# Performance work log

Measured on AMD Instinct MI355X. Metric: run time of the kernel, lower is better.

## Reference

```python
import jax, jax.numpy as jnp
import numpy as np

GRID_SIZE = 5
SPLINE_ORDER = 3
GRID_RANGE = (-1.0, 1.0)


def b_splines(x, grid, spline_order=SPLINE_ORDER):
    # x: [B, in], grid: [G] with G = grid_size + 2*spline_order + 1
    x = x[..., None]                      # [B, in, 1]
    g = grid[None, None, :]               # [1, 1, G]
    bases = ((x >= g[..., :-1]) & (x < g[..., 1:])).astype(x.dtype)  # [B, in, G-1]
    for k in range(1, spline_order + 1):
        left = (x - g[..., :-(k + 1)]) / (g[..., k:-1] - g[..., :-(k + 1)]) * bases[..., :-1]
        right = (g[..., k + 1:] - x) / (g[..., k + 1:] - g[..., 1:-k]) * bases[..., 1:]
        bases = left + right
    return bases                          # [B, in, grid_size + spline_order]


def setup_inputs() -> dict:
    key = jax.random.key(0)
    k1, k2, k3, k4 = jax.random.split(key, 4)
    B, IN, OUT = 32768, 256, 256
    n_coef = GRID_SIZE + SPLINE_ORDER  # 8
    h = (GRID_RANGE[1] - GRID_RANGE[0]) / GRID_SIZE
    grid = jnp.arange(-SPLINE_ORDER, GRID_SIZE + SPLINE_ORDER + 1, dtype=jnp.float32) * h + GRID_RANGE[0]  # [12]
    x = jax.random.normal(k1, (B, IN), dtype=jnp.float32)
    base_weight = jax.random.normal(k2, (OUT, IN), dtype=jnp.float32) * np.sqrt(2.0 / IN)
    spline_weight = jax.random.normal(k3, (OUT, IN, n_coef), dtype=jnp.float32) * (0.1 / GRID_SIZE)
    spline_scaler = jax.random.normal(k4, (OUT, IN), dtype=jnp.float32) * np.sqrt(2.0 / IN)
    return {"x": x, "base_weight": base_weight, "spline_weight": spline_weight,
            "spline_scaler": spline_scaler, "grid": grid}


def reference(x, base_weight, spline_weight, spline_scaler, grid):
    B = x.shape[0]
    out_features = base_weight.shape[0]
    # base branch: silu(x) @ base_weight^T
    base_out = jnp.matmul(jax.nn.silu(x), base_weight.T)  # [B, out]
    # spline branch
    bases = b_splines(x, grid)                             # [B, in, n_coef]
    scaled_w = spline_weight * spline_scaler[..., None]    # [out, in, n_coef]
    spline_out = jnp.matmul(bases.reshape(B, -1), scaled_w.reshape(out_features, -1).T)
    return base_out + spline_out
```

## Files before the change

kernel.cpp:

```cpp
#include <hip/hip_runtime.h>
#include <stdint.h>


#define IN_F 256
#define OUT_F 256
#define KDIM 2304
#define BK 64
#define NCHUNK (KDIM / BK)

typedef float f32x4 __attribute__((ext_vector_type(4)));
typedef short bf16x8 __attribute__((ext_vector_type(8)));

__device__ __forceinline__ uint32_t f2bf(float f) {
    union { float f; uint32_t u; } c; c.f = f;
    uint32_t u = c.u;
    return (u + 0x7FFFu + ((u >> 16) & 1u)) >> 16;
}

__device__ __forceinline__ uint32_t cvtpk(float lo, float hi) {
    uint32_t r;
    asm("v_cvt_pk_bf16_f32 %0, %1, %2" : "=v"(r) : "v"(lo), "v"(hi));
    return r;
}

__device__ __forceinline__ float silu_f(float v) {
    return v / (1.0f + __expf(-v));
}

__device__ __forceinline__ void block_sync_lds() {
    __builtin_amdgcn_sched_barrier(0);
    asm volatile("s_waitcnt lgkmcnt(0)" ::: "memory");
    __builtin_amdgcn_sched_barrier(0);
    __builtin_amdgcn_s_barrier();
    __builtin_amdgcn_sched_barrier(0);
}

__device__ __forceinline__ uint4 basis16(float xx) {
    float u = __builtin_fmaf(xx, 2.5f, 5.5f);
    float jf = floorf(u);
    float t = u - jf;
    int j0 = (int)jf;
    float t2 = t * t, t3 = t2 * t;
    float p3 = t3 * (1.0f / 6.0f);
    float p2 = __builtin_fmaf(t3, -0.5f,
               __builtin_fmaf(t2, 0.5f, __builtin_fmaf(t, 0.5f, 1.0f / 6.0f)));
    float p1 = __builtin_fmaf(t3, 0.5f, __builtin_fmaf(t2, -1.0f, 2.0f / 3.0f));
    float omt = 1.0f - t;
    float p0 = omt * omt * omt * (1.0f / 6.0f);
    const int s0 = j0 - 3;
    int ds = s0 >> 1;
    if ((unsigned)j0 > 10u) ds = 9;
    const bool odd = (s0 & 1) != 0;
    uint32_t v0 = cvtpk(odd ? 0.0f : p0, odd ? p0 : p1);
    uint32_t v1 = cvtpk(odd ? p1 : p2, odd ? p2 : p3);
    uint32_t v2 = odd ? cvtpk(p3, 0.0f) : 0u;
    uint4 r;
    r.x = (ds == 0) ? v0 : (ds == -1) ? v1 : (ds == -2) ? v2 : 0u;
    r.y = (ds == 1) ? v0 : (ds ==  0) ? v1 : (ds == -1) ? v2 : 0u;
    r.z = (ds == 2) ? v0 : (ds ==  1) ? v1 : (ds ==  0) ? v2 : 0u;
    r.w = (ds == 3) ? v0 : (ds ==  2) ? v1 : (ds ==  1) ? v2 : 0u;
    return r;
}

__device__ __forceinline__ size_t wcf_addr(int col, int k) {
    const int kc = k >> 6, kkh = (k >> 5) & 1, q = (k >> 3) & 3, e = k & 7;
    return ((size_t)((kc * 2 + kkh) * 16 + (col >> 4))) * 512 +
           (size_t)(q * 16 + (col & 15)) * 8 + e;
}

__global__ void build_w(const float* __restrict__ bw, const float* __restrict__ sw,
                        const float* __restrict__ ss, unsigned short* __restrict__ WcF) {
    const int o = blockIdx.x;
    const int i = threadIdx.x;
    WcF[wcf_addr(o, i)] = (unsigned short)f2bf(bw[o * IN_F + i]);
    const float scal = ss[o * IN_F + i];
    const float4* swv = reinterpret_cast<const float4*>(sw + (size_t)(o * IN_F + i) * 8);
    float4 s0 = swv[0], s1 = swv[1];
    uint4 wv;
    wv.x = f2bf(s0.x * scal) | (f2bf(s0.y * scal) << 16);
    wv.y = f2bf(s0.z * scal) | (f2bf(s0.w * scal) << 16);
    wv.z = f2bf(s1.x * scal) | (f2bf(s1.y * scal) << 16);
    wv.w = f2bf(s1.z * scal) | (f2bf(s1.w * scal) << 16);
    *reinterpret_cast<uint4*>(WcF + wcf_addr(o, IN_F + i * 8)) = wv;
}

__launch_bounds__(512, 2)
__global__ void kan_fused(const float* __restrict__ x, const unsigned short* __restrict__ WcF,
                          float* __restrict__ out) {
    __shared__ __align__(16) unsigned short As[4][64 * 64];

    const int bid = blockIdx.x;
    const int row0 = bid * 64;
    const int tid = threadIdx.x;
    const int lane = tid & 63;
    const int w = tid >> 6;
    const int kh = w >> 2;
    const int wn = w & 3;
    const int l15 = lane & 15;
    const int q = lane >> 4;

    const int erow = tid >> 3;
    const int g8   = tid & 7;

    f32x4 acc[4][4] = {};
    bf16x8 bE[4], bO[4];
    float x0, x1, x2, x3;

    const unsigned short* wbase = WcF + (size_t)lane * 8;

    auto load_b = [&](int kc, bf16x8* dst) {
#pragma unroll
        for (int nt = 0; nt < 4; ++nt)
            dst[nt] = *reinterpret_cast<const bf16x8*>(
                wbase + ((size_t)((kc * 2 + kh) * 16 + wn * 4 + nt)) * 512);
    };
    auto load_x_silu = [&](int c, float4& a, float4& b) {
        const float* xp = x + (size_t)(row0 + erow) * IN_F + c * 64 + g8 * 8;
        a = reinterpret_cast<const float4*>(xp)[0];
        b = reinterpret_cast<const float4*>(xp)[1];
    };
    auto load_x_bas = [&](int c, float& v) {
        v = x[(size_t)(row0 + erow) * IN_F + (c - 4) * 8 + g8];
    };
    auto expand_silu = [&](float4 a, float4 b, uint4& w0) {
        w0.x = cvtpk(silu_f(a.x), silu_f(a.y));
        w0.y = cvtpk(silu_f(a.z), silu_f(a.w));
        w0.z = cvtpk(silu_f(b.x), silu_f(b.y));
        w0.w = cvtpk(silu_f(b.z), silu_f(b.w));
    };
    auto write_a = [&](unsigned short* Ab, const uint4& w0) {
        *reinterpret_cast<uint4*>(Ab + erow * 64 + ((g8 ^ (erow & 7)) << 3)) = w0;
    };
    auto mfma_chunk = [&](const unsigned short* Ab, const bf16x8* bv) {
        const int g0 = kh * 4 + q;
#pragma unroll
        for (int mt = 0; mt < 4; ++mt) {
            int r = mt * 16 + l15;
            bf16x8 a = *reinterpret_cast<const bf16x8*>(
                Ab + r * 64 + ((g0 ^ (r & 7)) << 3));
            __builtin_amdgcn_s_setprio(1);
#pragma unroll
            for (int nt = 0; nt < 4; ++nt)
                acc[mt][nt] = __builtin_amdgcn_mfma_f32_16x16x32_bf16(
                    a, bv[nt], acc[mt][nt], 0, 0, 0);
            __builtin_amdgcn_s_setprio(0);
        }
    };

    float4 s2a, s2b, s3a, s3b;
    {
        float4 a, b; uint4 t;
        load_x_silu(0, a, b);
        load_x_silu(1, s2a, s2b);
        load_x_silu(2, s3a, s3b);
        load_b(0, bE);
        load_x_bas(4, x0);
        load_x_bas(5, x1);
        expand_silu(a, b, t);          write_a(&As[0][0], t);
        expand_silu(s2a, s2b, t);      write_a(&As[1][0], t);
        load_x_silu(3, s2a, s2b);
    }
    block_sync_lds();

    load_b(1, bO);
    {
        uint4 a2, a3;
        expand_silu(s3a, s3b, a2);
        expand_silu(s2a, s2b, a3);
        write_a(&As[2][0], a2);
        write_a(&As[3][0], a3);
    }
    mfma_chunk(&As[0][0], bE);
    load_b(2, bE);
    mfma_chunk(&As[1][0], bO);
    block_sync_lds();

    for (int t = 0; t < 8; ++t) {
        {
            const int kc = 4 * t + 2;
            load_b(kc + 1, bO);
            load_x_bas(kc + 4, x2);
            load_x_bas(kc + 5, x3);
            uint4 wa0, wa1;
            if (kh == 0) {
                wa0 = basis16(x0); wa1 = basis16(x1);
                write_a(&As[0][0], wa0); write_a(&As[1][0], wa1);
                mfma_chunk(&As[2][0], bE);
                load_b(kc + 2, bE);
                mfma_chunk(&As[3][0], bO);
            } else {
                mfma_chunk(&As[2][0], bE);
                load_b(kc + 2, bE);
                mfma_chunk(&As[3][0], bO);
                wa0 = basis16(x0); wa1 = basis16(x1);
                write_a(&As[0][0], wa0); write_a(&As[1][0], wa1);
            }
            block_sync_lds();
        }
        {
            const int kc2 = 4 * t + 4;
            load_b(kc2 + 1, bO);
            if (kc2 + 5 < NCHUNK) {
                load_x_bas(kc2 + 4, x0);
                load_x_bas(kc2 + 5, x1);
            }
            uint4 wa0, wa1;
            if (kh == 0) {
                wa0 = basis16(x2); wa1 = basis16(x3);
                write_a(&As[2][0], wa0); write_a(&As[3][0], wa1);
                mfma_chunk(&As[0][0], bE);
                load_b(kc2 + 2, bE);
                mfma_chunk(&As[1][0], bO);
            } else {
                mfma_chunk(&As[0][0], bE);
                load_b(kc2 + 2, bE);
                mfma_chunk(&As[1][0], bO);
                wa0 = basis16(x2); wa1 = basis16(x3);
                write_a(&As[2][0], wa0); write_a(&As[3][0], wa1);
            }
            block_sync_lds();
        }
    }

    load_b(35, bO);
    mfma_chunk(&As[2][0], bE);
    mfma_chunk(&As[3][0], bO);

    float* red = reinterpret_cast<float*>(&As[0][0]);
    const int slot = wn & 1;
    auto ridx = [&](int row, int col) {
        return row * 64 + (col ^ ((((row) >> 2) & 3) << 4));
    };
#pragma unroll
    for (int round = 0; round < 2; ++round) {
        block_sync_lds();
        if ((wn >> 1) == round && kh == 1) {
#pragma unroll
            for (int mt = 0; mt < 4; ++mt)
#pragma unroll
                for (int nt = 0; nt < 4; ++nt)
#pragma unroll
                    for (int r = 0; r < 4; ++r)
                        red[slot * 4096 + ridx(mt * 16 + q * 4 + r, nt * 16 + l15)] =
                            acc[mt][nt][r];
        }
        block_sync_lds();
        if ((wn >> 1) == round && kh == 0) {
#pragma unroll
            for (int mt = 0; mt < 4; ++mt)
#pragma unroll
                for (int nt = 0; nt < 4; ++nt)
#pragma unroll
                    for (int r = 0; r < 4; ++r) {
                        float v = acc[mt][nt][r] +
                                  red[slot * 4096 + ridx(mt * 16 + q * 4 + r, nt * 16 + l15)];
                        out[(size_t)(row0 + mt * 16 + q * 4 + r) * OUT_F +
                            wn * 64 + nt * 16 + l15] = v;
                    }
        }
    }
}

extern "C" void kernel_launch(void* const* d_in, const int* in_sizes, int n_in,
                              void* d_out, int out_size, void* d_ws, size_t ws_size,
                              hipStream_t stream) {
    const float* x  = (const float*)d_in[0];
    const float* bw = (const float*)d_in[1];
    const float* sw = (const float*)d_in[2];
    const float* ss = (const float*)d_in[3];
    unsigned short* WcF = (unsigned short*)d_ws;

    build_w<<<dim3(OUT_F), dim3(IN_F), 0, stream>>>(bw, sw, ss, WcF);

    const int B_ROWS = in_sizes[0] / IN_F;
    kan_fused<<<dim3(B_ROWS / 64), dim3(512), 0, stream>>>(
        x, WcF, (float*)d_out);
}
```

Before: 138.7 us.

## Build MFMA A-operands directly in registers instead of staging through LDS

Each lane now loads the x values matching its own MFMA A-fragment straight from global memory and computes the silu or B-spline basis in registers, then feeds the result to the MFMA. This removes the LDS staging buffers and the per-chunk block barriers. LDS is now used only for the final cross-wave reduction. In exchange, the 8 waves redundantly recompute overlapping basis and silu values and issue more scattered, smaller global loads of x.

```diff
diff --git a/kernel.cpp b/kernel.cpp
--- a/kernel.cpp
+++ b/kernel.cpp
@@ -87,7 +87,7 @@
 __launch_bounds__(512, 2)
 __global__ void kan_fused(const float* __restrict__ x, const unsigned short* __restrict__ WcF,
                           float* __restrict__ out) {
-    __shared__ __align__(16) unsigned short As[4][64 * 64];
+    __shared__ __align__(16) float red[2][64 * 64];
 
     const int bid = blockIdx.x;
     const int row0 = bid * 64;
@@ -99,14 +99,18 @@
     const int l15 = lane & 15;
     const int q = lane >> 4;
 
-    const int erow = tid >> 3;
-    const int g8   = tid & 7;
+    const int fOff = kh * 4 + q;
+    const int koff = fOff * 8;
 
     f32x4 acc[4][4] = {};
     bf16x8 bE[4], bO[4];
-    float x0, x1, x2, x3;
+    float xE[4], xO[4];
 
     const unsigned short* wbase = WcF + (size_t)lane * 8;
+    const float* xr[4];
+#pragma unroll
+    for (int mt = 0; mt < 4; ++mt)
+        xr[mt] = x + (size_t)(row0 + mt * 16 + l15) * IN_F;
 
     auto load_b = [&](int kc, bf16x8* dst) {
 #pragma unroll
@@ -114,122 +118,65 @@
             dst[nt] = *reinterpret_cast<const bf16x8*>(
                 wbase + ((size_t)((kc * 2 + kh) * 16 + wn * 4 + nt)) * 512);
     };
-    auto load_x_silu = [&](int c, float4& a, float4& b) {
-        const float* xp = x + (size_t)(row0 + erow) * IN_F + c * 64 + g8 * 8;
-        a = reinterpret_cast<const float4*>(xp)[0];
-        b = reinterpret_cast<const float4*>(xp)[1];
-    };
-    auto load_x_bas = [&](int c, float& v) {
-        v = x[(size_t)(row0 + erow) * IN_F + (c - 4) * 8 + g8];
-    };
-    auto expand_silu = [&](float4 a, float4 b, uint4& w0) {
-        w0.x = cvtpk(silu_f(a.x), silu_f(a.y));
-        w0.y = cvtpk(silu_f(a.z), silu_f(a.w));
-        w0.z = cvtpk(silu_f(b.x), silu_f(b.y));
-        w0.w = cvtpk(silu_f(b.z), silu_f(b.w));
-    };
-    auto write_a = [&](unsigned short* Ab, const uint4& w0) {
-        *reinterpret_cast<uint4*>(Ab + erow * 64 + ((g8 ^ (erow & 7)) << 3)) = w0;
-    };
-    auto mfma_chunk = [&](const unsigned short* Ab, const bf16x8* bv) {
-        const int g0 = kh * 4 + q;
+    auto load_x = [&](int c, float* xs) {
+#pragma unroll
+        for (int mt = 0; mt < 4; ++mt)
+            xs[mt] = xr[mt][(c - 4) * 8 + fOff];
+    };
+    auto mfma4 = [&](int mt, bf16x8 a, const bf16x8* bv) {
+        __builtin_amdgcn_s_setprio(1);
+#pragma unroll
+        for (int nt = 0; nt < 4; ++nt)
+            acc[mt][nt] = __builtin_amdgcn_mfma_f32_16x16x32_bf16(
+                a, bv[nt], acc[mt][nt], 0, 0, 0);
+        __builtin_amdgcn_s_setprio(0);
+    };
+
+    load_b(0, bE);
+    load_x(4, xE);
+#pragma unroll
+    for (int c = 0; c < 4; ++c) {
+        bf16x8* bcur = (c & 1) ? bO : bE;
+        bf16x8* bnxt = (c & 1) ? bE : bO;
+        load_b(c + 1, bnxt);
 #pragma unroll
         for (int mt = 0; mt < 4; ++mt) {
-            int r = mt * 16 + l15;
-            bf16x8 a = *reinterpret_cast<const bf16x8*>(
-                Ab + r * 64 + ((g0 ^ (r & 7)) << 3));
-            __builtin_amdgcn_s_setprio(1);
-#pragma unroll
-            for (int nt = 0; nt < 4; ++nt)
-                acc[mt][nt] = __builtin_amdgcn_mfma_f32_16x16x32_bf16(
-                    a, bv[nt], acc[mt][nt], 0, 0, 0);
-            __builtin_amdgcn_s_setprio(0);
-        }
-    };
-
-    float4 s2a, s2b, s3a, s3b;
-    {
-        float4 a, b; uint4 t;
-        load_x_silu(0, a, b);
-        load_x_silu(1, s2a, s2b);
-        load_x_silu(2, s3a, s3b);
-        load_b(0, bE);
-        load_x_bas(4, x0);
-        load_x_bas(5, x1);
-        expand_silu(a, b, t);          write_a(&As[0][0], t);
-        expand_silu(s2a, s2b, t);      write_a(&As[1][0], t);
-        load_x_silu(3, s2a, s2b);
+            const float* p = xr[mt] + c * 64 + koff;
+            float4 a = reinterpret_cast<const float4*>(p)[0];
+            float4 b = reinterpret_cast<const float4*>(p)[1];
+            uint4 wv;
+            wv.x = cvtpk(silu_f(a.x), silu_f(a.y));
+            wv.y = cvtpk(silu_f(a.z), silu_f(a.w));
+            wv.z = cvtpk(silu_f(b.x), silu_f(b.y));
+            wv.w = cvtpk(silu_f(b.z), silu_f(b.w));
+            mfma4(mt, *reinterpret_cast<bf16x8*>(&wv), bcur);
+        }
     }
-    block_sync_lds();
-
-    load_b(1, bO);
-    {
-        uint4 a2, a3;
-        expand_silu(s3a, s3b, a2);
-        expand_silu(s2a, s2b, a3);
-        write_a(&As[2][0], a2);
-        write_a(&As[3][0], a3);
+
+    for (int t = 0; t < 16; ++t) {
+        const int kc = 4 + 2 * t;
+        {
+            load_b(kc + 1, bO);
+            load_x(kc + 1, xO);
+#pragma unroll
+            for (int mt = 0; mt < 4; ++mt) {
+                uint4 fv = basis16(xE[mt]);
+                mfma4(mt, *reinterpret_cast<bf16x8*>(&fv), bE);
+            }
+        }
+        {
+            if (t < 15) { load_b(kc + 2, bE); load_x(kc + 2, xE); }
+#pragma unroll
+            for (int mt = 0; mt < 4; ++mt) {
+                uint4 fv = basis16(xO[mt]);
+                mfma4(mt, *reinterpret_cast<bf16x8*>(&fv), bO);
+            }
+        }
     }
-    mfma_chunk(&As[0][0], bE);
-    load_b(2, bE);
-    mfma_chunk(&As[1][0], bO);
-    block_sync_lds();
-
-    for (int t = 0; t < 8; ++t) {
-        {
-            const int kc = 4 * t + 2;
-            load_b(kc + 1, bO);
-            load_x_bas(kc + 4, x2);
-            load_x_bas(kc + 5, x3);
-            uint4 wa0, wa1;
-            if (kh == 0) {
-                wa0 = basis16(x0); wa1 = basis16(x1);
-                write_a(&As[0][0], wa0); write_a(&As[1][0], wa1);
-                mfma_chunk(&As[2][0], bE);
-                load_b(kc + 2, bE);
-                mfma_chunk(&As[3][0], bO);
-            } else {
-                mfma_chunk(&As[2][0], bE);
-                load_b(kc + 2, bE);
-                mfma_chunk(&As[3][0], bO);
-                wa0 = basis16(x0); wa1 = basis16(x1);
-                write_a(&As[0][0], wa0); write_a(&As[1][0], wa1);
-            }
-            block_sync_lds();
-        }
-        {
-            const int kc2 = 4 * t + 4;
-            load_b(kc2 + 1, bO);
-            if (kc2 + 5 < NCHUNK) {
-                load_x_bas(kc2 + 4, x0);
-                load_x_bas(kc2 + 5, x1);
-            }
-            uint4 wa0, wa1;
-            if (kh == 0) {
-                wa0 = basis16(x2); wa1 = basis16(x3);
-                write_a(&As[2][0], wa0); write_a(&As[3][0], wa1);
-                mfma_chunk(&As[0][0], bE);
-                load_b(kc2 + 2, bE);
-                mfma_chunk(&As[1][0], bO);
-            } else {
-                mfma_chunk(&As[0][0], bE);
-                load_b(kc2 + 2, bE);
-                mfma_chunk(&As[1][0], bO);
-                wa0 = basis16(x2); wa1 = basis16(x3);
-                write_a(&As[2][0], wa0); write_a(&As[3][0], wa1);
-            }
-            block_sync_lds();
-        }
-    }
-
-    load_b(35, bO);
-    mfma_chunk(&As[2][0], bE);
-    mfma_chunk(&As[3][0], bO);
-
-    float* red = reinterpret_cast<float*>(&As[0][0]);
+
     const int slot = wn & 1;
     auto ridx = [&](int row, int col) {
-        return row * 64 + (col ^ ((((row) >> 2) & 3) << 4));
+        return row * 64 + (col ^ (((row >> 2) & 3) << 4));
     };
 #pragma unroll
     for (int round = 0; round < 2; ++round) {
@@ -241,7 +188,7 @@
                 for (int nt = 0; nt < 4; ++nt)
 #pragma unroll
                     for (int r = 0; r < 4; ++r)
-                        red[slot * 4096 + ridx(mt * 16 + q * 4 + r, nt * 16 + l15)] =
+                        red[slot][ridx(mt * 16 + q * 4 + r, nt * 16 + l15)] =
                             acc[mt][nt][r];
         }
         block_sync_lds();
@@ -253,7 +200,7 @@
 #pragma unroll
                     for (int r = 0; r < 4; ++r) {
                         float v = acc[mt][nt][r] +
-                                  red[slot * 4096 + ridx(mt * 16 + q * 4 + r, nt * 16 + l15)];
+                                  red[slot][ridx(mt * 16 + q * 4 + r, nt * 16 + l15)];
                         out[(size_t)(row0 + mt * 16 + q * 4 + r) * OUT_F +
                             wn * 64 + nt * 16 + l15] = v;
                     }
```

Result: slower. 185.7 us (+33.9%).
